# Kernel tuning notes

Hardware: AMD Instinct MI355X
Metric: run time of the kernel (lower is better)

The kernel has to match this reference:

```python
import jax, jax.numpy as jnp
import numpy as np

HIDDEN = 768
HEADS = 12
NCH = 3

def setup_inputs() -> dict:
    key = jax.random.key(0)
    ks = jax.random.split(key, 8)
    B, S, D = 16, 512, HIDDEN
    Ht = jax.random.normal(ks[0], (B, S, D), dtype=jnp.float32)
    M_list = jax.random.uniform(ks[1], (B, NCH, S, S), dtype=jnp.float32)
    attention_mask = jnp.ones((B, S), dtype=jnp.float32)
    sc = 1.0 / np.sqrt(D)
    W_qk = jax.random.normal(ks[2], (D, 2 * D), dtype=jnp.float32) * sc
    b_qk = jnp.zeros((2 * D,), dtype=jnp.float32)
    W_gat = jax.random.normal(ks[3], (NCH, D, D), dtype=jnp.float32) * sc
    b_gat = jnp.zeros((NCH, D), dtype=jnp.float32)
    return {"Ht": Ht, "M_list": M_list, "attention_mask": attention_mask,
            "W_qk": W_qk, "b_qk": b_qk, "W_gat": W_gat, "b_gat": b_gat}

def reference(Ht, M_list, attention_mask, W_qk, b_qk, W_gat, b_gat):
    B, S, D = Ht.shape
    dh = D // HEADS
    # text self-attention
    qk = Ht @ W_qk + b_qk                                   # (B,S,2D)
    Q, K = jnp.split(qk, 2, axis=-1)
    Q = Q.reshape(B, S, HEADS, dh).transpose(0, 2, 1, 3)    # (B,H,S,dh)
    K = K.reshape(B, S, HEADS, dh).transpose(0, 2, 1, 3)
    scores = jnp.einsum('bhqd,bhkd->bhqk', Q, K) / jnp.sqrt(jnp.float32(D))
    scores = scores + (1.0 - attention_mask)[:, None, None, :] * (-1e9)
    P = jax.nn.softmax(scores, axis=-1)                     # (B,H,S,S)
    # pairwise mask
    mask_matrix = attention_mask[:, :, None] * attention_mask[:, None, :]  # (B,S,S)
    Mp = jnp.transpose(M_list, (1, 0, 2, 3))                # (h,B,S,S)
    feats = []
    for i in range(NCH):
        M = Mp[i] * mask_matrix                             # (B,S,S)
        A = M[:, None, :, :] * P                            # (B,H,S,S)
        A = A / (A.sum(axis=-1, keepdims=True) + 1e-10)
        feat = jnp.einsum('bqk,bkd->bqd', A.mean(axis=1), Ht)
        feat = jax.nn.relu(feat @ W_gat[i] + b_gat[i])      # (B,S,D)
        feats.append(feat * attention_mask[:, :, None])
    H_fusion = jnp.stack(feats).mean(axis=0)
    return H_fusion
```

## Files before the change

kernel.cpp:

```cpp
#include <hip/hip_runtime.h>
#include <math.h>

typedef __attribute__((ext_vector_type(8))) short short8;
typedef __attribute__((ext_vector_type(4))) float floatx4;

#define TB 16
#define TS 512
#define TD 768
#define TH 12
#define TDH 64
#define TNCH 3

#define SCALE 0.03608439182435161f

__device__ __forceinline__ unsigned short f2bf(float f) {
  unsigned u = __float_as_uint(f);
  u += 0x7fffu + ((u >> 16) & 1u);
  return (unsigned short)(u >> 16);
}
__device__ __forceinline__ unsigned f2bf2(float lo, float hi) {
  return (unsigned)f2bf(lo) | ((unsigned)f2bf(hi) << 16);
}

union U4 { uint4 u; short8 s; };

__global__ __launch_bounds__(256)
void pconv(const float* __restrict__ src, unsigned short* __restrict__ dst) {
  const int i = (blockIdx.x * 256 + threadIdx.x) * 8;
  const float4 a = *(const float4*)&src[i];
  const float4 b = *(const float4*)&src[i + 4];
  uint4 o;
  o.x = f2bf2(a.x, a.y); o.y = f2bf2(a.z, a.w);
  o.z = f2bf2(b.x, b.y); o.w = f2bf2(b.z, b.w);
  *(uint4*)&dst[i] = o;
}

__global__ __launch_bounds__(256)
void ptrans(const float* __restrict__ src, unsigned short* __restrict__ dst,
            int R, int C) {
  __shared__ float ts[32][33];
  const size_t zoff = (size_t)blockIdx.z * R * C;
  src += zoff; dst += zoff;
  const int c0 = blockIdx.x * 32, r0 = blockIdx.y * 32;
  const int x = threadIdx.x & 31, y = threadIdx.x >> 5;
#pragma unroll
  for (int i = 0; i < 4; i++)
    ts[y + 8 * i][x] = src[(size_t)(r0 + y + 8 * i) * C + c0 + x];
  __syncthreads();
#pragma unroll
  for (int i = 0; i < 4; i++)
    dst[(size_t)(c0 + y + 8 * i) * R + r0 + x] = f2bf(ts[x][y + 8 * i]);
}

__device__ __forceinline__ void stage_gll(const unsigned short* __restrict__ S, int ld,
                                          int row0, int k0, int w, int lane,
                                          unsigned short* D) {
  const int rsub = lane >> 2, c = lane & 3;
#pragma unroll
  for (int i = 0; i < 2; i++) {
    const int r = w * 32 + i * 16;
    const unsigned short* g = &S[(size_t)(row0 + r + rsub) * ld + k0 + c * 8];
    unsigned short* d = &D[r * 32];
    __builtin_amdgcn_global_load_lds(
        (const __attribute__((address_space(1))) unsigned int*)(const void*)g,
        (__attribute__((address_space(3))) unsigned int*)(void*)d,
        16, 0, 0);
  }
}

__device__ __forceinline__ void mfma_step_lin(const unsigned short* As, const unsigned short* Bs,
                                              int wy, int wx, int l16, int quad,
                                              floatx4 acc[4][4]) {
  short8 af[4], bfr[4];
#pragma unroll
  for (int i = 0; i < 4; i++) {
    U4 t; t.u = *(const uint4*)&As[(wy * 64 + i * 16 + l16) * 32 + quad * 8];
    af[i] = t.s;
  }
#pragma unroll
  for (int j = 0; j < 4; j++) {
    U4 t; t.u = *(const uint4*)&Bs[(wx * 64 + j * 16 + l16) * 32 + quad * 8];
    bfr[j] = t.s;
  }
#pragma unroll
  for (int i = 0; i < 4; i++)
#pragma unroll
    for (int j = 0; j < 4; j++)
      acc[i][j] = __builtin_amdgcn_mfma_f32_16x16x32_bf16(af[i], bfr[j], acc[i][j], 0, 0, 0);
}

__global__ __launch_bounds__(256, 2)
void k1_qk(const unsigned short* __restrict__ Htb, const unsigned short* __restrict__ WqkT,
           const float* __restrict__ bias, unsigned short* __restrict__ Q,
           unsigned short* __restrict__ Ko) {
  __shared__ unsigned short As[128 * 32];
  __shared__ unsigned short Bs[128 * 32];
  const int tid = threadIdx.x;
  const int row0 = blockIdx.y * 128, col0 = blockIdx.x * 128;
  const int w = tid >> 6, lane = tid & 63;
  const int wy = w >> 1, wx = w & 1, l16 = lane & 15, quad = lane >> 4;
  floatx4 acc[4][4];
#pragma unroll
  for (int i = 0; i < 4; i++)
#pragma unroll
    for (int j = 0; j < 4; j++)
#pragma unroll
      for (int r = 0; r < 4; r++) acc[i][j][r] = 0.f;

  for (int k0 = 0; k0 < TD; k0 += 32) {
    stage_gll(Htb, TD, row0, k0, w, lane, As);
    stage_gll(WqkT, TD, col0, k0, w, lane, Bs);
    __syncthreads();
    mfma_step_lin(As, Bs, wy, wx, l16, quad, acc);
    __syncthreads();
  }
#pragma unroll
  for (int i = 0; i < 4; i++)
#pragma unroll
    for (int j = 0; j < 4; j++) {
      const int col = col0 + wx * 64 + j * 16 + l16;
      const float bs = bias[col];
#pragma unroll
      for (int r = 0; r < 4; r++) {
        const int row = row0 + wy * 64 + i * 16 + quad * 4 + r;
        const float v = acc[i][j][r] + bs;
        if (col < TD) Q[(size_t)row * TD + col] = f2bf(v);
        else          Ko[(size_t)row * TD + (col - TD)] = f2bf(v);
      }
    }
}

#define OB_S 520
__global__ __launch_bounds__(256, 2)
void k2_attn(const unsigned short* __restrict__ Q, const unsigned short* __restrict__ Kb,
             const float* __restrict__ Ml, const float* __restrict__ am,
             unsigned short* __restrict__ Am) {
  __shared__ float4 ldsf4[1040];
  const int i0 = blockIdx.x;
  const int xcd = i0 & 7, jj = i0 >> 3;
  const int b = xcd + 8 * (jj & 1);
  const int q0 = (jj >> 1) * 16;
  const int tid = threadIdx.x;
  const int w = tid >> 6, lane = tid & 63;
  const int l16 = lane & 15, quad = lane >> 4;
  const int kbase = w * 128;

  const float* amb = am + b * TS;
  float amq[4], amk[8], maskv[8];
#pragma unroll
  for (int r = 0; r < 4; r++) amq[r] = amb[q0 + quad * 4 + r];
#pragma unroll
  for (int kt = 0; kt < 8; kt++) {
    amk[kt] = amb[kbase + kt * 16 + l16];
    maskv[kt] = (1.f - amk[kt]) * (-1e9f);
  }

  unsigned Mpk[TNCH][4][4];
#pragma unroll
  for (int i = 0; i < TNCH; i++)
#pragma unroll
    for (int r = 0; r < 4; r++) {
      const float* Mrow = Ml + ((size_t)((b * TNCH + i) * TS + q0 + quad * 4 + r)) * TS;
#pragma unroll
      for (int kt2 = 0; kt2 < 4; kt2++) {
        const int ke = kbase + kt2 * 32 + l16;
        const float me = Mrow[ke] * amk[kt2 * 2] * amq[r];
        const float mo = Mrow[ke + 16] * amk[kt2 * 2 + 1] * amq[r];
        Mpk[i][r][kt2] = f2bf2(me, mo);
      }
    }

  const unsigned short* qbase = Q + ((size_t)(b * TS + q0 + l16)) * TD + quad * 8;
  const unsigned short* kb0   = Kb + ((size_t)(b * TS + kbase + l16)) * TD + quad * 8;

  for (int h = 0; h < TH; h++) {
    floatx4 sacc[8];
#pragma unroll
    for (int kt = 0; kt < 8; kt++)
#pragma unroll
      for (int r = 0; r < 4; r++) sacc[kt][r] = 0.f;
#pragma unroll
    for (int dk = 0; dk < 2; dk++) {
      U4 a; a.u = *(const uint4*)(qbase + h * TDH + dk * 32);
#pragma unroll
      for (int kt = 0; kt < 8; kt++) {
        U4 bb; bb.u = *(const uint4*)(kb0 + (size_t)kt * 16 * TD + h * TDH + dk * 32);
        sacc[kt] = __builtin_amdgcn_mfma_f32_16x16x32_bf16(a.s, bb.s, sacc[kt], 0, 0, 0);
      }
    }
    float e[8][4];
    float Zp[4] = {0.f, 0.f, 0.f, 0.f};
#pragma unroll
    for (int kt = 0; kt < 8; kt++)
#pragma unroll
      for (int r = 0; r < 4; r++) {
        const float v = __expf(sacc[kt][r] * SCALE + maskv[kt]);
        e[kt][r] = v;
        Zp[r] += v;
      }
    float dmp[TNCH][4];
#pragma unroll
    for (int i = 0; i < TNCH; i++)
#pragma unroll
      for (int r = 0; r < 4; r++) {
        float d = 0.f;
#pragma unroll
        for (int kt2 = 0; kt2 < 4; kt2++) {
          const unsigned u = Mpk[i][r][kt2];
          d += __uint_as_float(u << 16) * e[kt2 * 2][r];
          d += __uint_as_float(u & 0xffff0000u) * e[kt2 * 2 + 1][r];
        }
        dmp[i][r] = d;
      }
#pragma unroll
    for (int r = 0; r < 4; r++) {
#pragma unroll
      for (int off = 1; off < 16; off <<= 1) {
        Zp[r] += __shfl_xor(Zp[r], off);
        dmp[0][r] += __shfl_xor(dmp[0][r], off);
        dmp[1][r] += __shfl_xor(dmp[1][r], off);
        dmp[2][r] += __shfl_xor(dmp[2][r], off);
      }
    }
    if (l16 == 0) {
#pragma unroll
      for (int r = 0; r < 4; r++)
        ldsf4[(h * 16 + quad * 4 + r) * 4 + w] =
            make_float4(Zp[r], dmp[0][r], dmp[1][r], dmp[2][r]);
    }
  }
  __syncthreads();

  if (tid < TH * 16) {
    const int h = tid >> 4, q = tid & 15;
    const int base = (h * 16 + q) * 4;
    const float4 p0 = ldsf4[base + 0];
    const float4 p1 = ldsf4[base + 1];
    const float4 p2 = ldsf4[base + 2];
    const float4 p3 = ldsf4[base + 3];
    const float Z  = p0.x + p1.x + p2.x + p3.x;
    const float d0 = p0.y + p1.y + p2.y + p3.y;
    const float d1 = p0.z + p1.z + p2.z + p3.z;
    const float d2 = p0.w + p1.w + p2.w + p3.w;
    const float ez = 1e-10f * Z + 1e-30f;
    ldsf4[768 + h * 16 + q] =
        make_float4(1.f / (d0 + ez), 1.f / (d1 + ez), 1.f / (d2 + ez), 0.f);
  }
  __syncthreads();

  float acc[TNCH][8][4];
#pragma unroll
  for (int i = 0; i < TNCH; i++)
#pragma unroll
    for (int kt = 0; kt < 8; kt++)
#pragma unroll
      for (int r = 0; r < 4; r++) acc[i][kt][r] = 0.f;

  for (int h = 0; h < TH; h++) {
    floatx4 sacc[8];
#pragma unroll
    for (int kt = 0; kt < 8; kt++)
#pragma unroll
      for (int r = 0; r < 4; r++) sacc[kt][r] = 0.f;
#pragma unroll
    for (int dk = 0; dk < 2; dk++) {
      U4 a; a.u = *(const uint4*)(qbase + h * TDH + dk * 32);
#pragma unroll
      for (int kt = 0; kt < 8; kt++) {
        U4 bb; bb.u = *(const uint4*)(kb0 + (size_t)kt * 16 * TD + h * TDH + dk * 32);
        sacc[kt] = __builtin_amdgcn_mfma_f32_16x16x32_bf16(a.s, bb.s, sacc[kt], 0, 0, 0);
      }
    }
    float4 wv[4];
#pragma unroll
    for (int r = 0; r < 4; r++) wv[r] = ldsf4[768 + h * 16 + quad * 4 + r];
#pragma unroll
    for (int kt = 0; kt < 8; kt++)
#pragma unroll
      for (int r = 0; r < 4; r++) {
        const float v = __expf(sacc[kt][r] * SCALE + maskv[kt]);
        acc[0][kt][r] += v * wv[r].x;
        acc[1][kt][r] += v * wv[r].y;
        acc[2][kt][r] += v * wv[r].z;
      }
  }
  __syncthreads();

  unsigned short* obuf = (unsigned short*)ldsf4;
  const float inv_h = 1.f / (float)TH;
  for (int i = 0; i < TNCH; i++) {
#pragma unroll
    for (int r = 0; r < 4; r++) {
      const int q = q0 + quad * 4 + r;
      const float* Mrow = Ml + ((size_t)((b * TNCH + i) * TS + q)) * TS;
#pragma unroll
      for (int kt = 0; kt < 8; kt++) {
        const int k = kbase + kt * 16 + l16;
        const float mv = Mrow[k] * amk[kt] * amq[r];
        obuf[(quad * 4 + r) * OB_S + k] = f2bf(mv * acc[i][kt][r] * inv_h);
      }
    }
    __syncthreads();
#pragma unroll
    for (int it = 0; it < 4; it++) {
      const int idx = tid + it * 256;
      const int row = idx >> 6, c16 = idx & 63;
      const uint4 v = *(const uint4*)&obuf[row * OB_S + c16 * 8];
      *(uint4*)&Am[((size_t)((i * TB + b) * TS + q0 + row)) * TS + c16 * 8] = v;
    }
    __syncthreads();
  }
}

__global__ __launch_bounds__(256, 2)
void k3_feat(const unsigned short* __restrict__ Am, const unsigned short* __restrict__ HtbT,
             unsigned short* __restrict__ G) {
  __shared__ unsigned short As[128 * 32];
  __shared__ unsigned short Bs[128 * 32];
  const int z = blockIdx.z;
  const int b = z & 15;
  const unsigned short* A  = Am + (size_t)z * TS * TS;
  const unsigned short* Bt = HtbT + (size_t)b * TD * TS;
  unsigned short* C = G + (size_t)z * TS * TD;
  const int tid = threadIdx.x;
  const int row0 = blockIdx.y * 128, col0 = blockIdx.x * 128;
  const int w = tid >> 6, lane = tid & 63;
  const int wy = w >> 1, wx = w & 1, l16 = lane & 15, quad = lane >> 4;
  floatx4 acc[4][4];
#pragma unroll
  for (int i = 0; i < 4; i++)
#pragma unroll
    for (int j = 0; j < 4; j++)
#pragma unroll
      for (int r = 0; r < 4; r++) acc[i][j][r] = 0.f;

  for (int k0 = 0; k0 < TS; k0 += 32) {
    stage_gll(A, TS, row0, k0, w, lane, As);
    stage_gll(Bt, TS, col0, k0, w, lane, Bs);
    __syncthreads();
    mfma_step_lin(As, Bs, wy, wx, l16, quad, acc);
    __syncthreads();
  }
#pragma unroll
  for (int i = 0; i < 4; i++)
#pragma unroll
    for (int j = 0; j < 4; j++) {
      const int col = col0 + wx * 64 + j * 16 + l16;
#pragma unroll
      for (int r = 0; r < 4; r++) {
        const int row = row0 + wy * 64 + i * 16 + quad * 4 + r;
        C[(size_t)row * TD + col] = f2bf(acc[i][j][r]);
      }
    }
}

__global__ __launch_bounds__(256, 2)
void k4_out(const unsigned short* __restrict__ G, const unsigned short* __restrict__ WgT,
            const float* __restrict__ bg, const float* __restrict__ am,
            float* __restrict__ out) {
  __shared__ unsigned short As[128 * 32];
  __shared__ unsigned short Bs[128 * 32];
  const int tid = threadIdx.x;
  const int row0 = blockIdx.y * 128, col0 = blockIdx.x * 128;
  const int w = tid >> 6, lane = tid & 63;
  const int wy = w >> 1, wx = w & 1, l16 = lane & 15, quad = lane >> 4;
  float osum[4][4][4];
#pragma unroll
  for (int i = 0; i < 4; i++)
#pragma unroll
    for (int j = 0; j < 4; j++)
#pragma unroll
      for (int r = 0; r < 4; r++) osum[i][j][r] = 0.f;

  for (int ch = 0; ch < TNCH; ch++) {
    const unsigned short* A  = G + (size_t)ch * (TB * TS) * TD;
    const unsigned short* Bt = WgT + (size_t)ch * TD * TD;
    floatx4 acc[4][4];
#pragma unroll
    for (int i = 0; i < 4; i++)
#pragma unroll
      for (int j = 0; j < 4; j++)
#pragma unroll
        for (int r = 0; r < 4; r++) acc[i][j][r] = 0.f;

    for (int k0 = 0; k0 < TD; k0 += 32) {
      stage_gll(A, TD, row0, k0, w, lane, As);
      stage_gll(Bt, TD, col0, k0, w, lane, Bs);
      __syncthreads();
      mfma_step_lin(As, Bs, wy, wx, l16, quad, acc);
      __syncthreads();
    }
#pragma unroll
    for (int i = 0; i < 4; i++)
#pragma unroll
      for (int j = 0; j < 4; j++) {
        const int col = col0 + wx * 64 + j * 16 + l16;
        const float bs = bg[ch * TD + col];
#pragma unroll
        for (int r = 0; r < 4; r++)
          osum[i][j][r] += fmaxf(acc[i][j][r] + bs, 0.f);
      }
  }
#pragma unroll
  for (int i = 0; i < 4; i++)
#pragma unroll
    for (int r = 0; r < 4; r++) {
      const int row = row0 + wy * 64 + i * 16 + quad * 4 + r;
      const float amr = am[row] * (1.f / 3.f);
#pragma unroll
      for (int j = 0; j < 4; j++) {
        const int col = col0 + wx * 64 + j * 16 + l16;
        out[(size_t)row * TD + col] = osum[i][j][r] * amr;
      }
    }
}

extern "C" void kernel_launch(void* const* d_in, const int* in_sizes, int n_in,
                              void* d_out, int out_size, void* d_ws, size_t ws_size,
                              hipStream_t stream) {
  const float* Ht    = (const float*)d_in[0];
  const float* Ml    = (const float*)d_in[1];
  const float* am    = (const float*)d_in[2];
  const float* W_qk  = (const float*)d_in[3];
  const float* b_qk  = (const float*)d_in[4];
  const float* W_gat = (const float*)d_in[5];
  const float* b_gat = (const float*)d_in[6];
  float* out = (float*)d_out;

  unsigned short* base = (unsigned short*)d_ws;
  const size_t SEG = (size_t)TB * TS * TD;
  unsigned short* Q    = base;
  unsigned short* Kw   = base + SEG;
  unsigned short* Htb  = base + 2 * SEG;
  unsigned short* HtbT = base + 3 * SEG;
  unsigned short* WqkT = base + 4 * SEG;
  unsigned short* WgT  = WqkT + (size_t)TD * 2 * TD;
  unsigned short* Am   = WgT + (size_t)TNCH * TD * TD;
  unsigned short* G    = base;

  pconv <<<dim3(3072), 256, 0, stream>>>(Ht, Htb);
  ptrans<<<dim3(24, 16, 16), 256, 0, stream>>>(Ht, HtbT, TS, TD);
  ptrans<<<dim3(48, 24, 1),  256, 0, stream>>>(W_qk, WqkT, TD, 2 * TD);
  ptrans<<<dim3(24, 24, 3),  256, 0, stream>>>(W_gat, WgT, TD, TD);

  k1_qk  <<<dim3(12, 64), 256, 0, stream>>>(Htb, WqkT, b_qk, Q, Kw);
  k2_attn<<<dim3(512), 256, 0, stream>>>(Q, Kw, Ml, am, Am);
  k3_feat<<<dim3(6, 4, 48), 256, 0, stream>>>(Am, HtbT, G);
  k4_out <<<dim3(6, 64), 256, 0, stream>>>(G, WgT, b_gat, am, out);
}
```

Measured before the change: 378.8 us.

## Split attention kernel over key halves into denominator and output kernels

The fused attention kernel is split into two kernels, each launched with twice as many blocks, and every block covers half of the keys. The first kernel writes per-half softmax and mask partial sums to global memory. The second kernel combines those partials, recomputes the scores and writes the normalized output. This raises parallelism and occupancy (launch bounds go from 2 to 4 blocks per SM) and lowers register pressure, at the cost of an extra launch, a global round-trip for the partials and recomputing the QK products once more per key half.

Measured after the change: 396.0 us. 4.6% more time.

```diff
diff --git a/kernel.cpp b/kernel.cpp
--- a/kernel.cpp
+++ b/kernel.cpp
@@ -130,39 +130,46 @@
     }
 }
 
-#define OB_S 520
-__global__ __launch_bounds__(256, 2)
-void k2_attn(const unsigned short* __restrict__ Q, const unsigned short* __restrict__ Kb,
+#define OB2 264
+
+__device__ __forceinline__ void k2_decomp(int i0, int& b, int& q0, int& ks) {
+  const int xcd = i0 & 7, j = i0 >> 3;
+  b = xcd + 8 * (j & 1);
+  const int j2 = j >> 1;
+  q0 = (j2 >> 1) * 16;
+  ks = j2 & 1;
+}
+
+__global__ __launch_bounds__(256, 4)
+void k2a_den(const unsigned short* __restrict__ Q, const unsigned short* __restrict__ Kb,
              const float* __restrict__ Ml, const float* __restrict__ am,
-             unsigned short* __restrict__ Am) {
-  __shared__ float4 ldsf4[1040];
-  const int i0 = blockIdx.x;
-  const int xcd = i0 & 7, jj = i0 >> 3;
-  const int b = xcd + 8 * (jj & 1);
-  const int q0 = (jj >> 1) * 16;
+             float4* __restrict__ part2) {
+  __shared__ float4 plds[TH][16][4];
+  int b, q0, ks;
+  k2_decomp(blockIdx.x, b, q0, ks);
   const int tid = threadIdx.x;
   const int w = tid >> 6, lane = tid & 63;
   const int l16 = lane & 15, quad = lane >> 4;
-  const int kbase = w * 128;
+  const int kbase = ks * 256 + w * 64;
 
   const float* amb = am + b * TS;
-  float amq[4], amk[8], maskv[8];
+  float amq[4], amk[4], maskv[4];
 #pragma unroll
   for (int r = 0; r < 4; r++) amq[r] = amb[q0 + quad * 4 + r];
 #pragma unroll
-  for (int kt = 0; kt < 8; kt++) {
+  for (int kt = 0; kt < 4; kt++) {
     amk[kt] = amb[kbase + kt * 16 + l16];
     maskv[kt] = (1.f - amk[kt]) * (-1e9f);
   }
 
-  unsigned Mpk[TNCH][4][4];
+  unsigned Mpk[TNCH][4][2];
 #pragma unroll
   for (int i = 0; i < TNCH; i++)
 #pragma unroll
     for (int r = 0; r < 4; r++) {
       const float* Mrow = Ml + ((size_t)((b * TNCH + i) * TS + q0 + quad * 4 + r)) * TS;
 #pragma unroll
-      for (int kt2 = 0; kt2 < 4; kt2++) {
+      for (int kt2 = 0; kt2 < 2; kt2++) {
         const int ke = kbase + kt2 * 32 + l16;
         const float me = Mrow[ke] * amk[kt2 * 2] * amq[r];
         const float mo = Mrow[ke + 16] * amk[kt2 * 2 + 1] * amq[r];
@@ -174,24 +181,24 @@
   const unsigned short* kb0   = Kb + ((size_t)(b * TS + kbase + l16)) * TD + quad * 8;
 
   for (int h = 0; h < TH; h++) {
-    floatx4 sacc[8];
-#pragma unroll
-    for (int kt = 0; kt < 8; kt++)
+    floatx4 sacc[4];
+#pragma unroll
+    for (int kt = 0; kt < 4; kt++)
 #pragma unroll
       for (int r = 0; r < 4; r++) sacc[kt][r] = 0.f;
 #pragma unroll
     for (int dk = 0; dk < 2; dk++) {
       U4 a; a.u = *(const uint4*)(qbase + h * TDH + dk * 32);
 #pragma unroll
-      for (int kt = 0; kt < 8; kt++) {
+      for (int kt = 0; kt < 4; kt++) {
         U4 bb; bb.u = *(const uint4*)(kb0 + (size_t)kt * 16 * TD + h * TDH + dk * 32);
         sacc[kt] = __builtin_amdgcn_mfma_f32_16x16x32_bf16(a.s, bb.s, sacc[kt], 0, 0, 0);
       }
     }
-    float e[8][4];
+    float e[4][4];
     float Zp[4] = {0.f, 0.f, 0.f, 0.f};
 #pragma unroll
-    for (int kt = 0; kt < 8; kt++)
+    for (int kt = 0; kt < 4; kt++)
 #pragma unroll
       for (int r = 0; r < 4; r++) {
         const float v = __expf(sacc[kt][r] * SCALE + maskv[kt]);
@@ -205,7 +212,7 @@
       for (int r = 0; r < 4; r++) {
         float d = 0.f;
 #pragma unroll
-        for (int kt2 = 0; kt2 < 4; kt2++) {
+        for (int kt2 = 0; kt2 < 2; kt2++) {
           const unsigned u = Mpk[i][r][kt2];
           d += __uint_as_float(u << 16) * e[kt2 * 2][r];
           d += __uint_as_float(u & 0xffff0000u) * e[kt2 * 2 + 1][r];
@@ -225,57 +232,93 @@
     if (l16 == 0) {
 #pragma unroll
       for (int r = 0; r < 4; r++)
-        ldsf4[(h * 16 + quad * 4 + r) * 4 + w] =
-            make_float4(Zp[r], dmp[0][r], dmp[1][r], dmp[2][r]);
+        plds[h][quad * 4 + r][w] = make_float4(Zp[r], dmp[0][r], dmp[1][r], dmp[2][r]);
     }
   }
   __syncthreads();
 
   if (tid < TH * 16) {
     const int h = tid >> 4, q = tid & 15;
-    const int base = (h * 16 + q) * 4;
-    const float4 p0 = ldsf4[base + 0];
-    const float4 p1 = ldsf4[base + 1];
-    const float4 p2 = ldsf4[base + 2];
-    const float4 p3 = ldsf4[base + 3];
-    const float Z  = p0.x + p1.x + p2.x + p3.x;
-    const float d0 = p0.y + p1.y + p2.y + p3.y;
-    const float d1 = p0.z + p1.z + p2.z + p3.z;
-    const float d2 = p0.w + p1.w + p2.w + p3.w;
+    const float4 p0 = plds[h][q][0];
+    const float4 p1 = plds[h][q][1];
+    const float4 p2 = plds[h][q][2];
+    const float4 p3 = plds[h][q][3];
+    part2[((size_t)(b * TH + h) * TS + q0 + q) * 2 + ks] =
+        make_float4((p0.x + p1.x) + (p2.x + p3.x),
+                    (p0.y + p1.y) + (p2.y + p3.y),
+                    (p0.z + p1.z) + (p2.z + p3.z),
+                    (p0.w + p1.w) + (p2.w + p3.w));
+  }
+}
+
+__global__ __launch_bounds__(256, 4)
+void k2c_out(const unsigned short* __restrict__ Q, const unsigned short* __restrict__ Kb,
+             const float* __restrict__ Ml, const float* __restrict__ am,
+             const float4* __restrict__ part2, unsigned short* __restrict__ Am) {
+  __shared__ float4 wlds[TH * 16];
+  __shared__ unsigned short obuf[16 * OB2];
+  int b, q0, ks;
+  k2_decomp(blockIdx.x, b, q0, ks);
+  const int tid = threadIdx.x;
+  const int w = tid >> 6, lane = tid & 63;
+  const int l16 = lane & 15, quad = lane >> 4;
+  const int kbase = ks * 256 + w * 64;
+
+  if (tid < TH * 16) {
+    const int h = tid >> 4, q = tid & 15;
+    const float4* p = &part2[((size_t)(b * TH + h) * TS + q0 + q) * 2];
+    const float4 v0 = p[0];
+    const float4 v1 = p[1];
+    const float Z  = v0.x + v1.x;
+    const float d0 = v0.y + v1.y;
+    const float d1 = v0.z + v1.z;
+    const float d2 = v0.w + v1.w;
     const float ez = 1e-10f * Z + 1e-30f;
-    ldsf4[768 + h * 16 + q] =
-        make_float4(1.f / (d0 + ez), 1.f / (d1 + ez), 1.f / (d2 + ez), 0.f);
+    wlds[h * 16 + q] = make_float4(1.f / (d0 + ez), 1.f / (d1 + ez), 1.f / (d2 + ez), 0.f);
   }
   __syncthreads();
 
-  float acc[TNCH][8][4];
+  const float* amb = am + b * TS;
+  float amq[4], amk[4], maskv[4];
+#pragma unroll
+  for (int r = 0; r < 4; r++) amq[r] = amb[q0 + quad * 4 + r];
+#pragma unroll
+  for (int kt = 0; kt < 4; kt++) {
+    amk[kt] = amb[kbase + kt * 16 + l16];
+    maskv[kt] = (1.f - amk[kt]) * (-1e9f);
+  }
+
+  const unsigned short* qbase = Q + ((size_t)(b * TS + q0 + l16)) * TD + quad * 8;
+  const unsigned short* kb0   = Kb + ((size_t)(b * TS + kbase + l16)) * TD + quad * 8;
+
+  float acc[TNCH][4][4];
 #pragma unroll
   for (int i = 0; i < TNCH; i++)
 #pragma unroll
-    for (int kt = 0; kt < 8; kt++)
+    for (int kt = 0; kt < 4; kt++)
 #pragma unroll
       for (int r = 0; r < 4; r++) acc[i][kt][r] = 0.f;
 
   for (int h = 0; h < TH; h++) {
-    floatx4 sacc[8];
-#pragma unroll
-    for (int kt = 0; kt < 8; kt++)
+    floatx4 sacc[4];
+#pragma unroll
+    for (int kt = 0; kt < 4; kt++)
 #pragma unroll
       for (int r = 0; r < 4; r++) sacc[kt][r] = 0.f;
 #pragma unroll
     for (int dk = 0; dk < 2; dk++) {
       U4 a; a.u = *(const uint4*)(qbase + h * TDH + dk * 32);
 #pragma unroll
-      for (int kt = 0; kt < 8; kt++) {
+      for (int kt = 0; kt < 4; kt++) {
         U4 bb; bb.u = *(const uint4*)(kb0 + (size_t)kt * 16 * TD + h * TDH + dk * 32);
         sacc[kt] = __builtin_amdgcn_mfma_f32_16x16x32_bf16(a.s, bb.s, sacc[kt], 0, 0, 0);
       }
     }
     float4 wv[4];
 #pragma unroll
-    for (int r = 0; r < 4; r++) wv[r] = ldsf4[768 + h * 16 + quad * 4 + r];
-#pragma unroll
-    for (int kt = 0; kt < 8; kt++)
+    for (int r = 0; r < 4; r++) wv[r] = wlds[h * 16 + quad * 4 + r];
+#pragma unroll
+    for (int kt = 0; kt < 4; kt++)
 #pragma unroll
       for (int r = 0; r < 4; r++) {
         const float v = __expf(sacc[kt][r] * SCALE + maskv[kt]);
@@ -284,31 +327,29 @@
         acc[2][kt][r] += v * wv[r].z;
       }
   }
-  __syncthreads();
-
-  unsigned short* obuf = (unsigned short*)ldsf4;
+
   const float inv_h = 1.f / (float)TH;
   for (int i = 0; i < TNCH; i++) {
+    __syncthreads();
 #pragma unroll
     for (int r = 0; r < 4; r++) {
       const int q = q0 + quad * 4 + r;
-      const float* Mrow = Ml + ((size_t)((b * TNCH + i) * TS + q)) * TS;
-#pragma unroll
-      for (int kt = 0; kt < 8; kt++) {
-        const int k = kbase + kt * 16 + l16;
-        const float mv = Mrow[k] * amk[kt] * amq[r];
-        obuf[(quad * 4 + r) * OB_S + k] = f2bf(mv * acc[i][kt][r] * inv_h);
-      }
-    }
-    __syncthreads();
-#pragma unroll
-    for (int it = 0; it < 4; it++) {
+      const float* Mrow = Ml + ((size_t)((b * TNCH + i) * TS + q)) * TS + ks * 256;
+#pragma unroll
+      for (int kt = 0; kt < 4; kt++) {
+        const int lc = w * 64 + kt * 16 + l16;
+        const float mv = Mrow[lc] * amk[kt] * amq[r];
+        obuf[(quad * 4 + r) * OB2 + lc] = f2bf(mv * acc[i][kt][r] * inv_h);
+      }
+    }
+    __syncthreads();
+#pragma unroll
+    for (int it = 0; it < 2; it++) {
       const int idx = tid + it * 256;
-      const int row = idx >> 6, c16 = idx & 63;
-      const uint4 v = *(const uint4*)&obuf[row * OB_S + c16 * 8];
-      *(uint4*)&Am[((size_t)((i * TB + b) * TS + q0 + row)) * TS + c16 * 8] = v;
-    }
-    __syncthreads();
+      const int row = idx >> 5, c16 = idx & 31;
+      const uint4 v = *(const uint4*)&obuf[row * OB2 + c16 * 8];
+      *(uint4*)&Am[((size_t)((i * TB + b) * TS + q0 + row)) * TS + ks * 256 + c16 * 8] = v;
+    }
   }
 }
 
@@ -437,6 +478,7 @@
   unsigned short* WgT  = WqkT + (size_t)TD * 2 * TD;
   unsigned short* Am   = WgT + (size_t)TNCH * TD * TD;
   unsigned short* G    = base;
+  float4* part2 = (float4*)(Am + (size_t)TNCH * TB * TS * TS);
 
   pconv <<<dim3(3072), 256, 0, stream>>>(Ht, Htb);
   ptrans<<<dim3(24, 16, 16), 256, 0, stream>>>(Ht, HtbT, TS, TD);
@@ -444,7 +486,8 @@
   ptrans<<<dim3(24, 24, 3),  256, 0, stream>>>(W_gat, WgT, TD, TD);
 
   k1_qk  <<<dim3(12, 64), 256, 0, stream>>>(Htb, WqkT, b_qk, Q, Kw);
-  k2_attn<<<dim3(512), 256, 0, stream>>>(Q, Kw, Ml, am, Am);
+  k2a_den<<<dim3(1024), 256, 0, stream>>>(Q, Kw, Ml, am, part2);
+  k2c_out<<<dim3(1024), 256, 0, stream>>>(Q, Kw, Ml, am, part2, Am);
   k3_feat<<<dim3(6, 4, 48), 256, 0, stream>>>(Am, HtbT, G);
   k4_out <<<dim3(6, 64), 256, 0, stream>>>(G, WgT, b_gat, am, out);
 }
```

## Retile output GEMM to 64x384 blocks with per-wave row strips

Applied to the files above, without the earlier changes.

The final projection kernel changes from 128x128 tiles split across a 2x2 wave grid to 64x384 tiles, where each wave owns a 16-row strip across all 384 columns. Each wave loads one A fragment per k-step and reuses it across 24 MFMAs, which cuts the number of A-side fetches. In exchange each wave holds far more accumulator registers, launch bounds drop to one block per SM, the grid shrinks from 384 to 256 blocks, and each k-step stages a much larger B tile.

Result: slower. 430.4 us (+13.6%).

```diff
diff --git a/kernel.cpp b/kernel.cpp
--- a/kernel.cpp
+++ b/kernel.cpp
@@ -354,65 +354,78 @@
     }
 }
 
-__global__ __launch_bounds__(256, 2)
+__global__ __launch_bounds__(256, 1)
 void k4_out(const unsigned short* __restrict__ G, const unsigned short* __restrict__ WgT,
             const float* __restrict__ bg, const float* __restrict__ am,
             float* __restrict__ out) {
-  __shared__ unsigned short As[128 * 32];
-  __shared__ unsigned short Bs[128 * 32];
+  __shared__ unsigned short As[64 * 32];
+  __shared__ unsigned short Bs[384 * 32];
   const int tid = threadIdx.x;
-  const int row0 = blockIdx.y * 128, col0 = blockIdx.x * 128;
   const int w = tid >> 6, lane = tid & 63;
-  const int wy = w >> 1, wx = w & 1, l16 = lane & 15, quad = lane >> 4;
-  float osum[4][4][4];
-#pragma unroll
-  for (int i = 0; i < 4; i++)
-#pragma unroll
-    for (int j = 0; j < 4; j++)
-#pragma unroll
-      for (int r = 0; r < 4; r++) osum[i][j][r] = 0.f;
+  const int l16 = lane & 15, quad = lane >> 4;
+  const int rsub = lane >> 2, cch = lane & 3;
+  const int row0 = blockIdx.y * 64;
+  const int col0 = blockIdx.x * 384;
+
+  float osum[24][4];
+#pragma unroll
+  for (int j = 0; j < 24; j++)
+#pragma unroll
+    for (int r = 0; r < 4; r++) osum[j][r] = 0.f;
 
   for (int ch = 0; ch < TNCH; ch++) {
     const unsigned short* A  = G + (size_t)ch * (TB * TS) * TD;
     const unsigned short* Bt = WgT + (size_t)ch * TD * TD;
-    floatx4 acc[4][4];
-#pragma unroll
-    for (int i = 0; i < 4; i++)
-#pragma unroll
-      for (int j = 0; j < 4; j++)
-#pragma unroll
-        for (int r = 0; r < 4; r++) acc[i][j][r] = 0.f;
+    floatx4 acc[24];
+#pragma unroll
+    for (int j = 0; j < 24; j++)
+#pragma unroll
+      for (int r = 0; r < 4; r++) acc[j][r] = 0.f;
 
     for (int k0 = 0; k0 < TD; k0 += 32) {
-      stage_gll(A, TD, row0, k0, w, lane, As);
-      stage_gll(Bt, TD, col0, k0, w, lane, Bs);
+      {
+        const unsigned short* g = &A[(size_t)(row0 + w * 16 + rsub) * TD + k0 + cch * 8];
+        __builtin_amdgcn_global_load_lds(
+            (const __attribute__((address_space(1))) unsigned int*)(const void*)g,
+            (__attribute__((address_space(3))) unsigned int*)(void*)&As[(w * 16) * 32],
+            16, 0, 0);
+      }
+#pragma unroll
+      for (int i = 0; i < 6; i++) {
+        const int r = i * 64 + w * 16;
+        const unsigned short* g = &Bt[(size_t)(col0 + r + rsub) * TD + k0 + cch * 8];
+        __builtin_amdgcn_global_load_lds(
+            (const __attribute__((address_space(1))) unsigned int*)(const void*)g,
+            (__attribute__((address_space(3))) unsigned int*)(void*)&Bs[r * 32],
+            16, 0, 0);
+      }
       __syncthreads();
-      mfma_step_lin(As, Bs, wy, wx, l16, quad, acc);
+      U4 a; a.u = *(const uint4*)&As[(w * 16 + l16) * 32 + quad * 8];
+#pragma unroll
+      for (int j = 0; j < 24; j++) {
+        U4 bb; bb.u = *(const uint4*)&Bs[(j * 16 + l16) * 32 + quad * 8];
+        acc[j] = __builtin_amdgcn_mfma_f32_16x16x32_bf16(a.s, bb.s, acc[j], 0, 0, 0);
+      }
       __syncthreads();
     }
 #pragma unroll
-    for (int i = 0; i < 4; i++)
-#pragma unroll
-      for (int j = 0; j < 4; j++) {
-        const int col = col0 + wx * 64 + j * 16 + l16;
-        const float bs = bg[ch * TD + col];
-#pragma unroll
-        for (int r = 0; r < 4; r++)
-          osum[i][j][r] += fmaxf(acc[i][j][r] + bs, 0.f);
-      }
-  }
-#pragma unroll
-  for (int i = 0; i < 4; i++)
-#pragma unroll
-    for (int r = 0; r < 4; r++) {
-      const int row = row0 + wy * 64 + i * 16 + quad * 4 + r;
-      const float amr = am[row] * (1.f / 3.f);
-#pragma unroll
-      for (int j = 0; j < 4; j++) {
-        const int col = col0 + wx * 64 + j * 16 + l16;
-        out[(size_t)row * TD + col] = osum[i][j][r] * amr;
-      }
-    }
+    for (int j = 0; j < 24; j++) {
+      const float bs = bg[ch * TD + col0 + j * 16 + l16];
+#pragma unroll
+      for (int r = 0; r < 4; r++)
+        osum[j][r] += fmaxf(acc[j][r] + bs, 0.f);
+    }
+  }
+#pragma unroll
+  for (int r = 0; r < 4; r++) {
+    const int row = row0 + w * 16 + quad * 4 + r;
+    const float amr = am[row] * (1.f / 3.f);
+#pragma unroll
+    for (int j = 0; j < 24; j++) {
+      const int col = col0 + j * 16 + l16;
+      out[(size_t)row * TD + col] = osum[j][r] * amr;
+    }
+  }
 }
 
 extern "C" void kernel_launch(void* const* d_in, const int* in_sizes, int n_in,
@@ -446,5 +459,5 @@
   k1_qk  <<<dim3(12, 64), 256, 0, stream>>>(Htb, WqkT, b_qk, Q, Kw);
   k2_attn<<<dim3(512), 256, 0, stream>>>(Q, Kw, Ml, am, Am);
   k3_feat<<<dim3(6, 4, 48), 256, 0, stream>>>(Am, HtbT, G);
-  k4_out <<<dim3(6, 64), 256, 0, stream>>>(G, WgT, b_gat, am, out);
-}
+  k4_out <<<dim3(2, 128), 256, 0, stream>>>(G, WgT, b_gat, am, out);
+}
```
